# Kernel optimization log

Hardware: AMD Instinct MI355X
Metric: run time of the kernel (lower is better)

The kernel has to match this reference:

```python
import jax, jax.numpy as jnp
import numpy as np
from jax.experimental.ode import odeint

TIME_STEPS = 1.0
B, S, I, H, O = 256, 64, 256, 1024, 10


def setup_inputs() -> dict:
    key = jax.random.key(0)
    ks = jax.random.split(key, 8)
    s_fc = 1.0 / np.sqrt(I)   # PyTorch Linear default init bound
    s_out = 1.0 / np.sqrt(H)
    return {
        "x": jax.random.normal(ks[0], (B, S, I), jnp.float32),
        "W_fc": jax.random.uniform(ks[1], (H, I), jnp.float32, -s_fc, s_fc),
        "b_fc": jax.random.uniform(ks[2], (H,), jnp.float32, -s_fc, s_fc),
        "alpha": jax.random.normal(ks[3], (H,), jnp.float32),
        "beta": jax.random.normal(ks[4], (H,), jnp.float32),
        "gamma": jax.random.normal(ks[5], (H,), jnp.float32),
        "W_out": jax.random.uniform(ks[6], (O, H), jnp.float32, -s_out, s_out),
        "b_out": jax.random.uniform(ks[7], (O,), jnp.float32, -s_out, s_out),
    }


def _ode_func(h, t, x, W_fc, b_fc, alpha, beta, gamma):
    # piecewise-constant input: current_step = min(int(t // interval), S-1)
    seq_len = x.shape[1]
    interval = TIME_STEPS / seq_len
    step = jnp.minimum(jnp.floor_divide(t, interval).astype(jnp.int32), seq_len - 1)
    input_t = jax.lax.dynamic_index_in_dim(x, step, axis=1, keepdims=False)  # [B, I]
    act = jnp.tanh(input_t @ W_fc.T + b_fc + gamma * h)   # [B, H]
    return -alpha * h + beta * act


def reference(x, W_fc, b_fc, alpha, beta, gamma, W_out, b_out):
    batch, seq_len, _ = x.shape
    hidden = W_fc.shape[0]
    h0 = jnp.zeros((batch, hidden), x.dtype)
    t = jnp.linspace(0.0, TIME_STEPS, seq_len)
    # adaptive dopri5 (same family as torchdiffeq's default 'dopri5')
    hs = odeint(_ode_func, h0, t, x, W_fc, b_fc, alpha, beta, gamma)  # [S, B, H]
    h_final = hs[-1]
    return h_final @ W_out.T + b_out  # [B, O]
```

## Files before the change

### kernel.cpp

```cpp
#include <hip/hip_runtime.h>
#include <hip/hip_bf16.h>


#define NB 256
#define NS 64
#define NI 256
#define NH 1024
#define NO 10
#define NBH (NB * NH)
#define KSUB 1

typedef __attribute__((ext_vector_type(8))) short short8;
typedef __attribute__((ext_vector_type(4))) float f32x4;


__device__ __forceinline__ void split1(float v, unsigned short& h, unsigned short& l)
{
    __hip_bfloat16 bh = __float2bfloat16(v);
    float fh = __bfloat162float(bh);
    __hip_bfloat16 bl = __float2bfloat16(v - fh);
    h = __builtin_bit_cast(unsigned short, bh);
    l = __builtin_bit_cast(unsigned short, bl);
}

#define XT 1024
#define WT 64

__global__ __launch_bounds__(256) void split_kernel(
    const float* __restrict__ x, const float* __restrict__ Wfc,
    unsigned short* __restrict__ xhi, unsigned short* __restrict__ xlo,
    unsigned short* __restrict__ whi, unsigned short* __restrict__ wlo,
    const float* __restrict__ bout, float* __restrict__ out)
{
    const int bid = blockIdx.x;
    const int t   = threadIdx.x;
    if (bid >= XT + WT) {
        for (int c = t; c < NB * NO; c += 256) out[c] = bout[c % NO];
        return;
    }
    __shared__ unsigned short lhi[4096];
    __shared__ unsigned short llo[4096];

    const float* srcbase;
    size_t row_stride;
    unsigned short *dsth, *dstl;
    if (bid < XT) {
        const int s = bid >> 4, bq = bid & 15;
        srcbase    = x + ((size_t)(bq * 16) * NS + s) * NI;
        row_stride = (size_t)NS * NI;
        dsth = xhi + (size_t)bid * 4096;
        dstl = xlo + (size_t)bid * 4096;
    } else {
        const int wx = bid - XT;
        srcbase    = Wfc + (size_t)(wx * 16) * NI;
        row_stride = NI;
        dsth = whi + (size_t)wx * 4096;
        dstl = wlo + (size_t)wx * 4096;
    }

#pragma unroll
    for (int i = 0; i < 4; ++i) {
        const int flat = t + i * 256;
        const int row  = flat >> 6;
        const int kq   = flat & 63;
        float4 v = *(const float4*)(srcbase + (size_t)row * row_stride + kq * 4);
        ushort4 h4, l4;
        split1(v.x, h4.x, l4.x); split1(v.y, h4.y, l4.y);
        split1(v.z, h4.z, l4.z); split1(v.w, h4.w, l4.w);
        const int kc  = kq >> 3;
        const int g   = (kq >> 1) & 3;
        const int e0  = (kq & 1) * 4;
        const int o   = (kc << 9) | (g << 7) | (row << 3) | e0;
        const int osw = o ^ (g << 2) ^ (kc << 3);
        *(ushort4*)&lhi[osw] = h4;
        *(ushort4*)&llo[osw] = l4;
    }
    __syncthreads();
#pragma unroll
    for (int i = 0; i < 2; ++i) {
        const int ob  = i * 2048 + t * 8;
        const int kc  = ob >> 9;
        const int g   = (ob >> 7) & 3;
        const int sw  = (g << 2) ^ (kc << 3);
        ushort4 a = *(const ushort4*)&lhi[ob ^ sw];
        ushort4 b = *(const ushort4*)&lhi[(ob + 4) ^ sw];
        *(ushort4*)(dsth + ob)     = a;
        *(ushort4*)(dsth + ob + 4) = b;
        ushort4 c4 = *(const ushort4*)&llo[ob ^ sw];
        ushort4 d4 = *(const ushort4*)&llo[(ob + 4) ^ sw];
        *(ushort4*)(dstl + ob)     = c4;
        *(ushort4*)(dstl + ob + 4) = d4;
    }
}

#define BM 128
#define BN 128
#define BK 32
#define KT 24

#define GLD16(gp, lp) __builtin_amdgcn_global_load_lds( \
    (const __attribute__((address_space(1))) unsigned int*)(gp), \
    (__attribute__((address_space(3))) unsigned int*)(lp), 16, 0, 0)

__global__ __launch_bounds__(256, 4) void fc_gemm_mfma(
    const unsigned short* __restrict__ Ahi, const unsigned short* __restrict__ Alo,
    const unsigned short* __restrict__ Whi, const unsigned short* __restrict__ Wlo,
    const float* __restrict__ bfc, float* __restrict__ U)
{
    __shared__ __hip_bfloat16 lA[2][8][4][16][8];
    __shared__ __hip_bfloat16 lB[2][8][4][16][8];

    const int t    = threadIdx.x;
    const int w    = t >> 6;
    const int lane = t & 63;
    const int wid  = ((blockIdx.x & 7) << 7) | (blockIdx.x >> 3);
    const int m16b = (wid >> 3) * 8;
    const int n16b = (wid & 7) * 8;
    const int m0   = m16b * 16;
    const int n0   = n16b * 16;
    const int row  = lane & 15;
    const int g    = lane >> 4;

    f32x4 acc[4][4];
#pragma unroll
    for (int i = 0; i < 4; ++i)
#pragma unroll
        for (int j = 0; j < 4; ++j) acc[i][j] = (f32x4){0.f, 0.f, 0.f, 0.f};

    auto stage = [&](int buf, int kt) {
        const unsigned short* As = (kt < 16) ? Ahi : Alo;
        const unsigned short* Bs = (kt < 8) ? Whi : ((kt < 16) ? Wlo : Whi);
        const int kc = kt & 7;
        const int ms = 2 * w;
        const unsigned short* ga0 = As + (((size_t)(m16b + ms) * 8 + kc) << 9) + lane * 8;
        const unsigned short* gb0 = Bs + (((size_t)(n16b + ms) * 8 + kc) << 9) + lane * 8;
        GLD16(ga0,        &lA[buf][ms][0][0][0]);
        GLD16(ga0 + 4096, &lA[buf][ms + 1][0][0][0]);
        GLD16(gb0,        &lB[buf][ms][0][0][0]);
        GLD16(gb0 + 4096, &lB[buf][ms + 1][0][0][0]);
    };

    const int wm = w >> 1, wn = w & 1;

    auto compute = [&](int buf) {
        short8 af[4], bfr[4];
#pragma unroll
        for (int f = 0; f < 4; ++f)
            af[f] = *(const short8*)((const short*)&lA[buf][wm * 4 + f][0][0][0] + lane * 8);
#pragma unroll
        for (int f = 0; f < 4; ++f)
            bfr[f] = *(const short8*)((const short*)&lB[buf][wn * 4 + f][0][0][0] + lane * 8);
#pragma unroll
        for (int fm = 0; fm < 4; ++fm)
#pragma unroll
            for (int fn = 0; fn < 4; ++fn)
                acc[fm][fn] = __builtin_amdgcn_mfma_f32_16x16x32_bf16(
                    af[fm], bfr[fn], acc[fm][fn], 0, 0, 0);
    };

    stage(0, 0);
    __syncthreads();
#pragma unroll 2
    for (int kt = 0; kt < KT; ++kt) {
        const int cur = kt & 1;
        if (kt + 1 < KT) stage(cur ^ 1, kt + 1);
        compute(cur);
        __syncthreads();
    }

    float* ep = (w < 2) ? (float*)lA + w * 1088 : (float*)lB + (w - 2) * 1088;
    float bias[4];
#pragma unroll
    for (int fn = 0; fn < 4; ++fn)
        bias[fn] = bfc[n0 + wn * 64 + fn * 16 + row];

#pragma unroll
    for (int fm = 0; fm < 4; ++fm) {
#pragma unroll
        for (int fn = 0; fn < 4; ++fn)
#pragma unroll
            for (int r = 0; r < 4; ++r)
                ep[(g * 4 + r) * 68 + fn * 16 + row] = acc[fm][fn][r] + bias[fn];
        asm volatile("s_waitcnt lgkmcnt(0)" ::: "memory");
        __builtin_amdgcn_sched_barrier(0);
#pragma unroll
        for (int k = 0; k < 4; ++k) {
            const int rl = 4 * k + g;
            float4 v = *(const float4*)&ep[rl * 68 + row * 4];
            const size_t gm = (size_t)(m0 + wm * 64 + fm * 16 + rl);
            *(float4*)&U[gm * NH + n0 + wn * 64 + row * 4] = v;
        }
        asm volatile("s_waitcnt lgkmcnt(0)" ::: "memory");
        __builtin_amdgcn_sched_barrier(0);
    }
}

__device__ __forceinline__ float f_eval(float h, float c, float d,
                                        float na, float be, float nbe2)
{
    float z2 = fmaf(c, h, d);
#if __has_builtin(__builtin_amdgcn_exp2f)
    float e = __builtin_amdgcn_exp2f(z2);
#else
    float e = __expf(0.69314718056f * z2);
#endif
    float r = __builtin_amdgcn_rcpf(e + 1.0f);
    return fmaf(nbe2, r, fmaf(na, h, be));
}

__global__ __launch_bounds__(128) void ode_out(
    const float* __restrict__ U, const float* __restrict__ alpha,
    const float* __restrict__ beta, const float* __restrict__ gamma,
    const float* __restrict__ Wout, float* __restrict__ out)
{
    const int k  = blockIdx.x;
    const int t  = threadIdx.x;
    const int b  = k >> 3;
    const int hh = (k & 7) * 128 + t;
    const int idx = b * NH + hh;

    const float na   = -alpha[hh];
    const float be   = beta[hh];
    const float nbe2 = -2.0f * be;
    const float L2E2 = 2.8853900817779268f;
    const float c   = L2E2 * gamma[hh];
    const float dt  = 1.0f / (float)(NS * KSUB);
    const float hdt = 0.5f * dt;
    const float dt6 = dt * (1.0f / 6.0f);

    float h = 0.f;
    float u[8];
#pragma unroll
    for (int j = 0; j < 8; ++j)
        u[j] = U[(size_t)j * NBH + idx];

#pragma unroll 1
    for (int sc = 0; sc < 8; ++sc) {
        const int s0 = sc * 8;
#pragma unroll
        for (int j = 0; j < 8; ++j) {
            const float d = L2E2 * u[j];
            float k1 = f_eval(h, c, d, na, be, nbe2);
            float k2 = f_eval(fmaf(hdt, k1, h), c, d, na, be, nbe2);
            float k3 = f_eval(fmaf(hdt, k2, h), c, d, na, be, nbe2);
            float k4 = f_eval(fmaf(dt, k3, h), c, d, na, be, nbe2);
            float t1 = k2 + k3;
            float t2 = k1 + k4;
            h = fmaf(dt6, fmaf(2.0f, t1, t2), h);
            const int sp = (s0 + j + 8 < NS) ? s0 + j + 8 : NS - 1;
            u[j] = U[(size_t)sp * NBH + idx];
        }
    }

    __shared__ float red[2][NO];
    const int wid2 = t >> 6, lane = t & 63;
#pragma unroll
    for (int o = 0; o < NO; ++o) {
        float p = h * Wout[(size_t)o * NH + hh];
#pragma unroll
        for (int off = 32; off > 0; off >>= 1)
            p += __shfl_down(p, off, 64);
        if (lane == 0) red[wid2][o] = p;
    }
    __syncthreads();
    if (t < NO)
        atomicAdd(&out[b * NO + t], red[0][t] + red[1][t]);
}

extern "C" void kernel_launch(void* const* d_in, const int* in_sizes, int n_in,
                              void* d_out, int out_size, void* d_ws, size_t ws_size,
                              hipStream_t stream)
{
    const float* x     = (const float*)d_in[0];
    const float* Wfc   = (const float*)d_in[1];
    const float* bfc   = (const float*)d_in[2];
    const float* alpha = (const float*)d_in[3];
    const float* beta  = (const float*)d_in[4];
    const float* gamma = (const float*)d_in[5];
    const float* Wout  = (const float*)d_in[6];
    const float* bout  = (const float*)d_in[7];
    float* out = (float*)d_out;

    float* U = (float*)d_ws;
    unsigned short* xhi = (unsigned short*)(U + (size_t)NS * NB * NH);
    unsigned short* xlo = xhi + (size_t)NS * NB * NI;
    unsigned short* whi = xlo + (size_t)NS * NB * NI;
    unsigned short* wlo = whi + (size_t)NH * NI;

    split_kernel<<<XT + WT + 1, 256, 0, stream>>>(
        x, Wfc, xhi, xlo, whi, wlo, bout, out);

    fc_gemm_mfma<<<(NH / BN) * ((NS * NB) / BM), 256, 0, stream>>>(
        xhi, xlo, whi, wlo, bfc, U);

    ode_out<<<(NB * NH) / 128, 128, 0, stream>>>(U, alpha, beta, gamma, Wout, out);
}
```

Baseline: 158.8 us.

## Fuse input-projection GEMM into ODE integration kernel with register-resident weights

Replaces the separate MFMA GEMM, which wrote the full [S,B,H] projection U to global memory, and the ODE kernel that read it back, with a single fused kernel. Each block keeps a 16-batch by 64-hidden tile of W_fc's hi/lo bf16 split in registers, computes that timestep's projection with MFMAs, and immediately runs the RK4 step. Input slices are streamed into a 6-deep LDS ring using global_load_lds with explicit vmcnt waits. This removes the 64 MB U round-trip and one launch, at the cost of a serialized per-step GEMM, only 256 blocks at occupancy 1, and two barriers per timestep.

```diff
diff --git a/kernel.cpp b/kernel.cpp
--- a/kernel.cpp
+++ b/kernel.cpp
@@ -7,8 +7,6 @@
 #define NI 256
 #define NH 1024
 #define NO 10
-#define NBH (NB * NH)
-#define KSUB 1
 
 typedef __attribute__((ext_vector_type(8))) short short8;
 typedef __attribute__((ext_vector_type(4))) float f32x4;
@@ -93,107 +91,11 @@
     }
 }
 
-#define BM 128
-#define BN 128
-#define BK 32
-#define KT 24
+#define RING 6
 
 #define GLD16(gp, lp) __builtin_amdgcn_global_load_lds( \
     (const __attribute__((address_space(1))) unsigned int*)(gp), \
     (__attribute__((address_space(3))) unsigned int*)(lp), 16, 0, 0)
-
-__global__ __launch_bounds__(256, 4) void fc_gemm_mfma(
-    const unsigned short* __restrict__ Ahi, const unsigned short* __restrict__ Alo,
-    const unsigned short* __restrict__ Whi, const unsigned short* __restrict__ Wlo,
-    const float* __restrict__ bfc, float* __restrict__ U)
-{
-    __shared__ __hip_bfloat16 lA[2][8][4][16][8];
-    __shared__ __hip_bfloat16 lB[2][8][4][16][8];
-
-    const int t    = threadIdx.x;
-    const int w    = t >> 6;
-    const int lane = t & 63;
-    const int wid  = ((blockIdx.x & 7) << 7) | (blockIdx.x >> 3);
-    const int m16b = (wid >> 3) * 8;
-    const int n16b = (wid & 7) * 8;
-    const int m0   = m16b * 16;
-    const int n0   = n16b * 16;
-    const int row  = lane & 15;
-    const int g    = lane >> 4;
-
-    f32x4 acc[4][4];
-#pragma unroll
-    for (int i = 0; i < 4; ++i)
-#pragma unroll
-        for (int j = 0; j < 4; ++j) acc[i][j] = (f32x4){0.f, 0.f, 0.f, 0.f};
-
-    auto stage = [&](int buf, int kt) {
-        const unsigned short* As = (kt < 16) ? Ahi : Alo;
-        const unsigned short* Bs = (kt < 8) ? Whi : ((kt < 16) ? Wlo : Whi);
-        const int kc = kt & 7;
-        const int ms = 2 * w;
-        const unsigned short* ga0 = As + (((size_t)(m16b + ms) * 8 + kc) << 9) + lane * 8;
-        const unsigned short* gb0 = Bs + (((size_t)(n16b + ms) * 8 + kc) << 9) + lane * 8;
-        GLD16(ga0,        &lA[buf][ms][0][0][0]);
-        GLD16(ga0 + 4096, &lA[buf][ms + 1][0][0][0]);
-        GLD16(gb0,        &lB[buf][ms][0][0][0]);
-        GLD16(gb0 + 4096, &lB[buf][ms + 1][0][0][0]);
-    };
-
-    const int wm = w >> 1, wn = w & 1;
-
-    auto compute = [&](int buf) {
-        short8 af[4], bfr[4];
-#pragma unroll
-        for (int f = 0; f < 4; ++f)
-            af[f] = *(const short8*)((const short*)&lA[buf][wm * 4 + f][0][0][0] + lane * 8);
-#pragma unroll
-        for (int f = 0; f < 4; ++f)
-            bfr[f] = *(const short8*)((const short*)&lB[buf][wn * 4 + f][0][0][0] + lane * 8);
-#pragma unroll
-        for (int fm = 0; fm < 4; ++fm)
-#pragma unroll
-            for (int fn = 0; fn < 4; ++fn)
-                acc[fm][fn] = __builtin_amdgcn_mfma_f32_16x16x32_bf16(
-                    af[fm], bfr[fn], acc[fm][fn], 0, 0, 0);
-    };
-
-    stage(0, 0);
-    __syncthreads();
-#pragma unroll 2
-    for (int kt = 0; kt < KT; ++kt) {
-        const int cur = kt & 1;
-        if (kt + 1 < KT) stage(cur ^ 1, kt + 1);
-        compute(cur);
-        __syncthreads();
-    }
-
-    float* ep = (w < 2) ? (float*)lA + w * 1088 : (float*)lB + (w - 2) * 1088;
-    float bias[4];
-#pragma unroll
-    for (int fn = 0; fn < 4; ++fn)
-        bias[fn] = bfc[n0 + wn * 64 + fn * 16 + row];
-
-#pragma unroll
-    for (int fm = 0; fm < 4; ++fm) {
-#pragma unroll
-        for (int fn = 0; fn < 4; ++fn)
-#pragma unroll
-            for (int r = 0; r < 4; ++r)
-                ep[(g * 4 + r) * 68 + fn * 16 + row] = acc[fm][fn][r] + bias[fn];
-        asm volatile("s_waitcnt lgkmcnt(0)" ::: "memory");
-        __builtin_amdgcn_sched_barrier(0);
-#pragma unroll
-        for (int k = 0; k < 4; ++k) {
-            const int rl = 4 * k + g;
-            float4 v = *(const float4*)&ep[rl * 68 + row * 4];
-            const size_t gm = (size_t)(m0 + wm * 64 + fm * 16 + rl);
-            *(float4*)&U[gm * NH + n0 + wn * 64 + row * 4] = v;
-        }
-        asm volatile("s_waitcnt lgkmcnt(0)" ::: "memory");
-        __builtin_amdgcn_sched_barrier(0);
-    }
-}
 
 __device__ __forceinline__ float f_eval(float h, float c, float d,
                                         float na, float be, float nbe2)
@@ -208,63 +110,124 @@
     return fmaf(nbe2, r, fmaf(na, h, be));
 }
 
-__global__ __launch_bounds__(128) void ode_out(
-    const float* __restrict__ U, const float* __restrict__ alpha,
+__global__ __launch_bounds__(256, 1) void fused_ode(
+    const unsigned short* __restrict__ xhi, const unsigned short* __restrict__ xlo,
+    const unsigned short* __restrict__ whi, const unsigned short* __restrict__ wlo,
+    const float* __restrict__ bfc, const float* __restrict__ alpha,
     const float* __restrict__ beta, const float* __restrict__ gamma,
     const float* __restrict__ Wout, float* __restrict__ out)
 {
-    const int k  = blockIdx.x;
-    const int t  = threadIdx.x;
-    const int b  = k >> 3;
-    const int hh = (k & 7) * 128 + t;
-    const int idx = b * NH + hh;
-
+    __shared__ unsigned short ring[RING][2][8][512];
+    __shared__ float red[4][4][4][NO];
+
+    const int t    = threadIdx.x;
+    const int w    = t >> 6;
+    const int lane = t & 63;
+    const int g    = lane >> 4;
+    const int col  = lane & 15;
+    const int bid  = blockIdx.x;
+    const int bq = (bid & 7) * 2 + ((bid >> 3) >> 4);
+    const int hb = (bid >> 3) & 15;
+    const int hh = hb * 64 + w * 16 + col;
+
+    short8 wh[8], wl[8];
+    const size_t wbase = (size_t)(hb * 4 + w) * 4096 + lane * 8;
+#pragma unroll
+    for (int kc = 0; kc < 8; ++kc) {
+        wh[kc] = *(const short8*)(whi + wbase + kc * 512);
+        wl[kc] = *(const short8*)(wlo + wbase + kc * 512);
+    }
+    const float bias = bfc[hh];
     const float na   = -alpha[hh];
     const float be   = beta[hh];
     const float nbe2 = -2.0f * be;
     const float L2E2 = 2.8853900817779268f;
-    const float c   = L2E2 * gamma[hh];
-    const float dt  = 1.0f / (float)(NS * KSUB);
-    const float hdt = 0.5f * dt;
-    const float dt6 = dt * (1.0f / 6.0f);
-
-    float h = 0.f;
-    float u[8];
-#pragma unroll
-    for (int j = 0; j < 8; ++j)
-        u[j] = U[(size_t)j * NBH + idx];
-
+    const float cg   = L2E2 * gamma[hh];
+    const float dt   = 1.0f / 64.0f;
+    const float hdt  = 0.5f * dt;
+    const float dt6  = dt * (1.0f / 6.0f);
+
+    auto stage = [&](int slot, int s) {
+        const size_t tb = (size_t)(s * 16 + bq) * 4096 + lane * 8;
+#pragma unroll
+        for (int q = 0; q < 4; ++q) {
+            const int id = w * 4 + q, part = id >> 3, kc = id & 7;
+            const unsigned short* src = (part ? xlo : xhi) + tb + kc * 512;
+            GLD16(src, &ring[slot][part][kc][0]);
+        }
+    };
+
+    float h4[4] = {0.f, 0.f, 0.f, 0.f};
+
+#pragma unroll
+    for (int s = 0; s < RING; ++s) stage(s, s);
+
+    int slot = 0;
 #pragma unroll 1
-    for (int sc = 0; sc < 8; ++sc) {
-        const int s0 = sc * 8;
-#pragma unroll
-        for (int j = 0; j < 8; ++j) {
-            const float d = L2E2 * u[j];
-            float k1 = f_eval(h, c, d, na, be, nbe2);
-            float k2 = f_eval(fmaf(hdt, k1, h), c, d, na, be, nbe2);
-            float k3 = f_eval(fmaf(hdt, k2, h), c, d, na, be, nbe2);
-            float k4 = f_eval(fmaf(dt, k3, h), c, d, na, be, nbe2);
-            float t1 = k2 + k3;
-            float t2 = k1 + k4;
-            h = fmaf(dt6, fmaf(2.0f, t1, t2), h);
-            const int sp = (s0 + j + 8 < NS) ? s0 + j + 8 : NS - 1;
-            u[j] = U[(size_t)sp * NBH + idx];
-        }
-    }
-
-    __shared__ float red[2][NO];
-    const int wid2 = t >> 6, lane = t & 63;
+    for (int s = 0; s < NS; ++s) {
+        if (s < NS - RING)       asm volatile("s_waitcnt vmcnt(20)" ::: "memory");
+        else if (s == NS - RING) asm volatile("s_waitcnt vmcnt(0)"  ::: "memory");
+        __builtin_amdgcn_sched_barrier(0);
+        __builtin_amdgcn_s_barrier();
+        __builtin_amdgcn_sched_barrier(0);
+
+        const unsigned short* Ah = &ring[slot][0][0][0];
+        const unsigned short* Al = &ring[slot][1][0][0];
+        f32x4 ac[4];
+#pragma unroll
+        for (int kc = 0; kc < 8; ++kc) {
+            short8 a = *(const short8*)(Ah + kc * 512 + lane * 8);
+            f32x4 c0 = (kc < 4) ? (f32x4){0.f, 0.f, 0.f, 0.f} : ac[kc & 3];
+            f32x4 tm = __builtin_amdgcn_mfma_f32_16x16x32_bf16(a, wh[kc], c0, 0, 0, 0);
+            ac[kc & 3] = __builtin_amdgcn_mfma_f32_16x16x32_bf16(a, wl[kc], tm, 0, 0, 0);
+        }
+#pragma unroll
+        for (int kc = 0; kc < 8; ++kc) {
+            short8 a = *(const short8*)(Al + kc * 512 + lane * 8);
+            ac[kc & 3] = __builtin_amdgcn_mfma_f32_16x16x32_bf16(a, wh[kc], ac[kc & 3], 0, 0, 0);
+        }
+        f32x4 us = (ac[0] + ac[1]) + (ac[2] + ac[3]);
+
+#pragma unroll
+        for (int r = 0; r < 4; ++r) {
+            const float d = L2E2 * (us[r] + bias);
+            float k1 = f_eval(h4[r], cg, d, na, be, nbe2);
+            float k2 = f_eval(fmaf(hdt, k1, h4[r]), cg, d, na, be, nbe2);
+            float k3 = f_eval(fmaf(hdt, k2, h4[r]), cg, d, na, be, nbe2);
+            float k4 = f_eval(fmaf(dt, k3, h4[r]), cg, d, na, be, nbe2);
+            h4[r] = fmaf(dt6, fmaf(2.0f, k2 + k3, k1 + k4), h4[r]);
+        }
+
+        __builtin_amdgcn_sched_barrier(0);
+        __builtin_amdgcn_s_barrier();
+        __builtin_amdgcn_sched_barrier(0);
+        if (s + RING < NS) stage(slot, s + RING);
+        ++slot; if (slot == RING) slot = 0;
+    }
+
 #pragma unroll
     for (int o = 0; o < NO; ++o) {
-        float p = h * Wout[(size_t)o * NH + hh];
-#pragma unroll
-        for (int off = 32; off > 0; off >>= 1)
-            p += __shfl_down(p, off, 64);
-        if (lane == 0) red[wid2][o] = p;
+        const float wv = Wout[(size_t)o * NH + hh];
+        float p0 = h4[0] * wv, p1 = h4[1] * wv, p2 = h4[2] * wv, p3 = h4[3] * wv;
+#pragma unroll
+        for (int m = 1; m < 16; m <<= 1) {
+            p0 += __shfl_xor(p0, m, 64);
+            p1 += __shfl_xor(p1, m, 64);
+            p2 += __shfl_xor(p2, m, 64);
+            p3 += __shfl_xor(p3, m, 64);
+        }
+        if (col == 0) {
+            red[w][g][0][o] = p0; red[w][g][1][o] = p1;
+            red[w][g][2][o] = p2; red[w][g][3][o] = p3;
+        }
     }
     __syncthreads();
-    if (t < NO)
-        atomicAdd(&out[b * NO + t], red[0][t] + red[1][t]);
+    if (t < 160) {
+        const int o  = t % NO, gr = t / NO;
+        const float sum = red[0][gr >> 2][gr & 3][o] + red[1][gr >> 2][gr & 3][o]
+                        + red[2][gr >> 2][gr & 3][o] + red[3][gr >> 2][gr & 3][o];
+        atomicAdd(&out[(bq * 16 + gr) * NO + o], sum);
+    }
 }
 
 extern "C" void kernel_launch(void* const* d_in, const int* in_sizes, int n_in,
@@ -281,8 +244,7 @@
     const float* bout  = (const float*)d_in[7];
     float* out = (float*)d_out;
 
-    float* U = (float*)d_ws;
-    unsigned short* xhi = (unsigned short*)(U + (size_t)NS * NB * NH);
+    unsigned short* xhi = (unsigned short*)d_ws;
     unsigned short* xlo = xhi + (size_t)NS * NB * NI;
     unsigned short* whi = xlo + (size_t)NS * NB * NI;
     unsigned short* wlo = whi + (size_t)NH * NI;
@@ -290,8 +252,6 @@
     split_kernel<<<XT + WT + 1, 256, 0, stream>>>(
         x, Wfc, xhi, xlo, whi, wlo, bout, out);
 
-    fc_gemm_mfma<<<(NH / BN) * ((NS * NB) / BM), 256, 0, stream>>>(
-        xhi, xlo, whi, wlo, bfc, U);
-
-    ode_out<<<(NB * NH) / 128, 128, 0, stream>>>(U, alpha, beta, gamma, Wout, out);
-}
+    fused_ode<<<NB, 256, 0, stream>>>(
+        xhi, xlo, whi, wlo, bfc, alpha, beta, gamma, Wout, out);
+}
```

Result: faster. 136.9 us (-13.7%).
